# Performance work log

Measured on AMD Instinct MI355X. Metric: run time of the kernel, lower is better.

## Reference

```python
import jax, jax.numpy as jnp
import numpy as np

B, N_PIC, C, H, W, P = 32, 4, 3, 224, 224, 16
HP = H // P  # 14
NP = HP * HP  # 196 patches
D = C * P * P  # 768 = hidden_size


def setup_inputs() -> dict:
    key = jax.random.key(0)
    ks = jax.random.split(key, 12)
    s = 0.02
    def lin(k, din, dout):
        kw, kb = jax.random.split(k)
        return (jax.random.normal(kw, (din, dout), jnp.float32) * s,
                jax.random.normal(kb, (dout,), jnp.float32) * s)
    W1, b1 = lin(ks[0], D, D)
    Wq, bq = lin(ks[1], D, D)
    Wk, bk = lin(ks[2], D, D)
    Wv, bv = lin(ks[3], D, D)
    Wo1, bo1 = lin(ks[4], D, D)
    Wo2, bo2 = lin(ks[5], D, D)
    x = jax.random.normal(ks[6], (B, N_PIC, C, H, W), jnp.float32)
    return {"x": x, "W1": W1, "b1": b1, "Wq": Wq, "bq": bq, "Wk": Wk,
            "bk": bk, "Wv": Wv, "bv": bv, "Wo1": Wo1, "bo1": bo1,
            "Wo2": Wo2, "bo2": bo2}


def reference(x, W1, b1, Wq, bq, Wk, bk, Wv, bv, Wo1, bo1, Wo2, bo2):
    b = x.shape[0]
    # patchify: matches torch unfold(3,P,P).unfold(4,P,P) + permute + view
    # -> [b, N, num_patches, C*P*P] with (C, ph, pw) ordering in last dim
    p = x.reshape(b, N_PIC, C, HP, P, HP, P)
    p = p.transpose(0, 1, 3, 5, 2, 4, 6).reshape(b, N_PIC, NP, D)
    h = p @ W1 + b1  # [b, N, S, D]
    # attention: query always from picture 0; key/value per picture (batched)
    Q = h[:, 0] @ Wq + bq          # [b, S, D]
    K = h @ Wk + bk                # [b, N, S, D]
    V = h @ Wv + bv                # [b, N, S, D]
    scale = 1.0 / jnp.sqrt(jnp.float32(D))
    scores = jnp.einsum('bsd,bnmd->bnsm', Q, K) * scale  # [b, N, S, S]
    attn = jax.nn.softmax(scores, axis=-1)
    wv = jnp.einsum('bnsm,bnmd->bnsd', attn, V)           # [b, N, S, D]
    out = jax.nn.relu(wv @ Wo1 + bo1) @ Wo2 + bo2
    return out
```

## Files before the change

kernel.cpp:

```cpp
#include <hip/hip_runtime.h>

typedef __bf16 bf16;
typedef __bf16 bf16x8 __attribute__((ext_vector_type(8)));
typedef float  f32x4  __attribute__((ext_vector_type(4)));


__global__ __launch_bounds__(256) void patchify_k(const float* __restrict__ x,
                                                  bf16* __restrict__ p) {
  int t = blockIdx.x * 256 + threadIdx.x;
  if (t >= 128 * 3 * 14 * 16 * 14) return;
  int j  = t % 14; t /= 14;
  int ph = t % 16; t /= 16;
  int i  = t % 14; t /= 14;
  int c  = t % 3;  t /= 3;
  int bn = t;
  const float* src = x + (((long long)(bn * 3 + c) * 224 + (i * 16 + ph)) * 224 + j * 16);
  bf16* dst = p + ((long long)(bn * 196 + (i * 14 + j)) * 768 + c * 256 + ph * 16);
  bf16 tmp[16];
  for (int k = 0; k < 16; k += 4) {
    float4 f = *(const float4*)(src + k);
    tmp[k + 0] = (bf16)f.x; tmp[k + 1] = (bf16)f.y;
    tmp[k + 2] = (bf16)f.z; tmp[k + 3] = (bf16)f.w;
  }
  *(bf16x8*)(dst)     = *(bf16x8*)&tmp[0];
  *(bf16x8*)(dst + 8) = *(bf16x8*)&tmp[8];
}

__global__ __launch_bounds__(256) void wtrans_k(const float* __restrict__ w0,
                                                const float* __restrict__ w1,
                                                const float* __restrict__ w2,
                                                const float* __restrict__ w3,
                                                const float* __restrict__ w4,
                                                const float* __restrict__ w5,
                                                bf16* __restrict__ out) {
  __shared__ float tile[32][33];
  const float* W;
  switch (blockIdx.z) {
    case 0: W = w0; break; case 1: W = w1; break; case 2: W = w2; break;
    case 3: W = w3; break; case 4: W = w4; break; default: W = w5; break;
  }
  bf16* o = out + (long long)blockIdx.z * 768 * 768;
  int nb = blockIdx.x * 32, kb = blockIdx.y * 32;
  int c = threadIdx.x & 31, r = threadIdx.x >> 5;
  for (int rr = 0; rr < 32; rr += 8)
    tile[r + rr][c] = W[(long long)(kb + r + rr) * 768 + nb + c];
  __syncthreads();
  for (int rr = 0; rr < 32; rr += 8)
    o[(long long)(nb + r + rr) * 768 + kb + c] = (bf16)tile[c][r + rr];
}

__global__ __launch_bounds__(256) void vtrans_k(const bf16* __restrict__ kv,
                                                bf16* __restrict__ Vt) {
  __shared__ short tile[32][33];
  int z = blockIdx.z;
  const short* v = (const short*)(kv + (long long)z * 301056 + 768);
  short* vt = (short*)(Vt + (long long)z * 768 * 224);
  int db = blockIdx.x * 32;
  int mb = blockIdx.y * 32;
  int c = threadIdx.x & 31, r = threadIdx.x >> 5;
  for (int rr = 0; rr < 32; rr += 8) {
    int m = mb + r + rr;
    short val = 0;
    if (m < 196) val = v[(long long)m * 1536 + db + c];
    tile[r + rr][c] = val;
  }
  __syncthreads();
  for (int rr = 0; rr < 32; rr += 8) {
    int d = db + r + rr;
    vt[(long long)d * 224 + mb + c] = tile[c][r + rr];
  }
}

__global__ __launch_bounds__(64) void softmax_k(const float* __restrict__ S,
                                                bf16* __restrict__ attn) {
  const int row = blockIdx.x;
  const float* sr = S + (long long)row * 196;
  const int l = threadIdx.x;
  float v0 = sr[l];
  float v1 = sr[l + 64];
  float v2 = sr[l + 128];
  float v3 = (l + 192 < 196) ? sr[l + 192] : -1e30f;
  float mx = fmaxf(fmaxf(v0, v1), fmaxf(v2, v3));
  for (int o = 32; o > 0; o >>= 1) mx = fmaxf(mx, __shfl_xor(mx, o));
  float e0 = __expf(v0 - mx);
  float e1 = __expf(v1 - mx);
  float e2 = __expf(v2 - mx);
  float e3 = (l + 192 < 196) ? __expf(v3 - mx) : 0.f;
  float s = e0 + e1 + e2 + e3;
  for (int o = 32; o > 0; o >>= 1) s += __shfl_xor(s, o);
  float inv = 1.0f / s;
  bf16* ar = attn + (long long)row * 224;
  ar[l]       = (bf16)(e0 * inv);
  ar[l + 64]  = (bf16)(e1 * inv);
  ar[l + 128] = (bf16)(e2 * inv);
  int m3 = l + 192;
  if (m3 < 196) ar[m3] = (bf16)(e3 * inv);
  else if (m3 < 224) ar[m3] = (bf16)0.0f;
}

__device__ __forceinline__ void gld16(const bf16* g, bf16* l) {
  __builtin_amdgcn_global_load_lds(
      (const __attribute__((address_space(1))) unsigned int*)g,
      (__attribute__((address_space(3))) unsigned int*)l, 16, 0, 0);
}

__global__ __launch_bounds__(256) void gemm128(
    const bf16* __restrict__ A, const bf16* __restrict__ Bt,
    const float* __restrict__ bias, const float* __restrict__ bias2,
    void* __restrict__ Cout,
    int M, int N, int K, int lda, int ldb, int gr, long long gs,
    long long strideAz, int a_zdiv, long long strideBz, long long strideCz,
    float scale, int relu, int out_bf16) {
  __shared__ __align__(16) char smem[34816];
  bf16* AsBuf = (bf16*)smem;
  bf16* BsBuf = (bf16*)(smem + 16384);

  const int tid = threadIdx.x;
  const int lane = tid & 63;
  const int w = tid >> 6;
  const int wm = w & 1, wn = w >> 1;
  const int z = blockIdx.z;
  const int n0 = blockIdx.x * 128, m0 = blockIdx.y * 128;

  const bf16* Az  = A  + (long long)(z / a_zdiv) * strideAz;
  const bf16* Btz = Bt + (long long)z * strideBz;

  const int rl  = 16 * w + (lane & 15);
  const int kc8 = (lane >> 4) * 8;
  int ar0 = m0 + rl;        if (ar0 >= M) ar0 = M - 1;
  int ar1 = m0 + 64 + rl;   if (ar1 >= M) ar1 = M - 1;
  const bf16* aP0 = Az + (long long)(ar0 / gr) * gs + (long long)(ar0 % gr) * lda + kc8;
  const bf16* aP1 = Az + (long long)(ar1 / gr) * gs + (long long)(ar1 % gr) * lda + kc8;
  int br0 = n0 + rl;        if (br0 >= N) br0 = N - 1;
  int br1 = n0 + 64 + rl;   if (br1 >= N) br1 = N - 1;
  const bf16* bP0 = Btz + (long long)br0 * ldb + kc8;
  const bf16* bP1 = Btz + (long long)br1 * ldb + kc8;

  const int dstOff = w * 512;

#define ISSUE(t, buf) do { const int _o = (t) << 5;                 \
    gld16(aP0 + _o, AsBuf + (buf) * 4096 + dstOff);                 \
    gld16(aP1 + _o, AsBuf + (buf) * 4096 + 2048 + dstOff);          \
    gld16(bP0 + _o, BsBuf + (buf) * 4096 + dstOff);                 \
    gld16(bP1 + _o, BsBuf + (buf) * 4096 + 2048 + dstOff); } while (0)

  const int niter = K >> 5;
  f32x4 acc[4][4] = {};
  const int fr = lane & 15, fq = lane >> 4;

  ISSUE(0, 0);

  for (int i = 0; i < niter; ++i) {
    __syncthreads();
    const int cur = i & 1;
    if (i + 1 < niter) ISSUE(i + 1, cur ^ 1);

    const bf16* Ac = AsBuf + cur * 4096;
    const bf16* Bc = BsBuf + cur * 4096;
    bf16x8 a[4], b[4];
#pragma unroll
    for (int mi = 0; mi < 4; mi++)
      a[mi] = *(const bf16x8*)&Ac[(wm * 4 + mi) * 512 + fq * 128 + fr * 8];
#pragma unroll
    for (int ni = 0; ni < 4; ni++)
      b[ni] = *(const bf16x8*)&Bc[(wn * 4 + ni) * 512 + fq * 128 + fr * 8];
#pragma unroll
    for (int mi = 0; mi < 4; mi++)
#pragma unroll
      for (int ni = 0; ni < 4; ni++)
        acc[mi][ni] = __builtin_amdgcn_mfma_f32_16x16x32_bf16(a[mi], b[ni], acc[mi][ni], 0, 0, 0);
  }
#undef ISSUE

  __syncthreads();

  const long long cz = (long long)z * strideCz;
  if (out_bf16) {
    bf16* Cs = (bf16*)smem;
#pragma unroll
    for (int ni = 0; ni < 4; ni++) {
      int col = wn * 64 + ni * 16 + fr;
      int gcol = n0 + col;
      float bb = 0.f;
      if (bias) bb = (bias2 && gcol >= 768) ? bias2[gcol - 768] : bias[gcol];
#pragma unroll
      for (int mi = 0; mi < 4; mi++) {
        int rbase = wm * 64 + mi * 16 + fq * 4;
#pragma unroll
        for (int r = 0; r < 4; r++) {
          float v = acc[mi][ni][r] * scale + bb;
          if (relu) v = fmaxf(v, 0.f);
          Cs[(rbase + r) * 136 + col] = (bf16)v;
        }
      }
    }
    __syncthreads();
    bf16* Cp = (bf16*)Cout;
    const int rr = tid >> 4, cc = (tid & 15) * 8;
#pragma unroll
    for (int pp = 0; pp < 8; pp++) {
      int row = pp * 16 + rr;
      int grow = m0 + row;
      if (grow < M)
        *(bf16x8*)(Cp + cz + (long long)grow * N + n0 + cc) =
            *(const bf16x8*)&Cs[row * 136 + cc];
    }
  } else {
    float* Cs = (float*)smem;
    float* Cp = (float*)Cout;
    for (int half = 0; half < 2; ++half) {
      if (wm == half) {
#pragma unroll
        for (int ni = 0; ni < 4; ni++) {
          int col = wn * 64 + ni * 16 + fr;
          int gcol = n0 + col;
          float bb = 0.f;
          if (bias && gcol < N)
            bb = (bias2 && gcol >= 768) ? bias2[gcol - 768] : bias[gcol];
#pragma unroll
          for (int mi = 0; mi < 4; mi++) {
            int rbase = mi * 16 + fq * 4;
#pragma unroll
            for (int r = 0; r < 4; r++) {
              float v = acc[mi][ni][r] * scale + bb;
              if (relu) v = fmaxf(v, 0.f);
              Cs[(rbase + r) * 132 + col] = v;
            }
          }
        }
      }
      __syncthreads();
      const int rr = tid >> 5, cc = (tid & 31) * 4;
#pragma unroll
      for (int pp = 0; pp < 8; pp++) {
        int row = pp * 8 + rr;
        int grow = m0 + half * 64 + row;
        if (grow < M) {
          int gcol = n0 + cc;
          float* dst = Cp + cz + (long long)grow * N + gcol;
          const float* srcl = &Cs[row * 132 + cc];
          if (gcol + 4 <= N) {
            *(float4*)dst = *(const float4*)srcl;
          } else {
            for (int e = 0; e < 4; e++)
              if (gcol + e < N) dst[e] = srcl[e];
          }
        }
      }
      __syncthreads();
    }
  }
}

__global__ __launch_bounds__(512, 2) void gemm256(
    const bf16* __restrict__ A, const bf16* __restrict__ Bt,
    const float* __restrict__ bias, const float* __restrict__ bias2,
    void* __restrict__ Cout,
    int N, int K, int lda, int ldb, int relu, int out_bf16) {
  __shared__ __align__(16) char smem[131072];
  bf16* As = (bf16*)smem;
  bf16* Bs = (bf16*)(smem + 65536);

  const int tid = threadIdx.x;
  const int lane = tid & 63;
  const int w = tid >> 6;
  const int wm = w >> 2;
  const int wn = w & 3;

  const int nx = N >> 8;
  const int nwg = gridDim.x * gridDim.y;
  int f = blockIdx.y * gridDim.x + blockIdx.x;
  {
    const int q = nwg >> 3, r = nwg & 7;
    const int xcd = f & 7, idx = f >> 3;
    f = (xcd < r ? xcd * (q + 1) : r * (q + 1) + (xcd - r) * q) + idx;
  }
  const int n0 = (f % nx) * 256;
  const int m0 = (f / nx) * 256;

  const int srow = ((tid >> 2) & 15) + ((tid >> 7) << 4);
  const int scol = ((tid >> 6) & 1) * 32 +
                   (((tid & 3) << 3) ^ ((tid & 32) ? 16 : 0));
  const bf16* aBase = A  + (long long)(m0 + srow) * lda + scol;
  const bf16* bBase = Bt + (long long)(n0 + srow) * ldb + scol;
  const int ldsw = w * 512;

#define STGQ(base, ld, dstArr, buf, kt, hh, q)                               \
  gld16((base) + (long long)((hh) * 128 + (q) * 64) * (ld) + (kt) * 64,      \
        (dstArr) + (buf) * 16384 + (hh) * 8192 + (q) * 4096 + ldsw)

  const int fr = lane & 15, fq = lane >> 4;
  const int frij = fr * 32 + ((fq * 8) ^ ((fr & 8) ? 16 : 0));
  const bf16* aRd = As + wm * 8192 + frij;
  const bf16* bRd = Bs + (wn >> 1) * 8192 + (wn & 1) * 4096 + frij;

  f32x4 acc[8][4] = {};
  bf16x8 A0f[4][2], A1f[4][2], B0f[2][2], B1f[2][2];

  const int nt = K >> 6;

  STGQ(aBase, lda, As, 0, 0, 0, 0); STGQ(aBase, lda, As, 0, 0, 1, 0);
  STGQ(bBase, ldb, Bs, 0, 0, 1, 0); STGQ(bBase, ldb, Bs, 0, 0, 1, 1);
  STGQ(aBase, lda, As, 0, 0, 0, 1); STGQ(aBase, lda, As, 0, 0, 1, 1);
  STGQ(bBase, ldb, Bs, 0, 0, 0, 0); STGQ(bBase, ldb, Bs, 0, 0, 0, 1);
  STGQ(aBase, lda, As, 1, 1, 0, 0); STGQ(aBase, lda, As, 1, 1, 1, 0);
  STGQ(bBase, ldb, Bs, 1, 1, 1, 0); STGQ(bBase, ldb, Bs, 1, 1, 1, 1);
  STGQ(aBase, lda, As, 1, 1, 0, 1); STGQ(aBase, lda, As, 1, 1, 1, 1);
  STGQ(bBase, ldb, Bs, 1, 1, 0, 0); STGQ(bBase, ldb, Bs, 1, 1, 0, 1);
  asm volatile("s_waitcnt vmcnt(8)" ::: "memory");
  asm volatile("s_barrier" ::: "memory");
#pragma unroll
  for (int mi = 0; mi < 4; ++mi)
#pragma unroll
    for (int kk = 0; kk < 2; ++kk)
      A0f[mi][kk] = *(const bf16x8*)(aRd + mi * 1024 + kk * 512);
#pragma unroll
  for (int ni = 0; ni < 2; ++ni)
#pragma unroll
    for (int kk = 0; kk < 2; ++kk)
      B0f[ni][kk] = *(const bf16x8*)(bRd + ni * 1024 + kk * 512);
  asm volatile("s_waitcnt lgkmcnt(0)" ::: "memory");
  __builtin_amdgcn_sched_barrier(0);
  asm volatile("s_barrier" ::: "memory");

  for (int t = 0; t < nt; ++t) {
    const int bo = (t & 1) << 14;
    const int bn = ((t & 1) ^ 1) << 14;
    const int b = t & 1;
    const bool stg = (t + 2 < nt);
    const bool nxt = (t + 1 < nt);

#pragma unroll
    for (int ni = 0; ni < 2; ++ni)
#pragma unroll
      for (int kk = 0; kk < 2; ++kk)
        B1f[ni][kk] = *(const bf16x8*)(bRd + bo + (2 + ni) * 1024 + kk * 512);
    if (stg) { STGQ(aBase, lda, As, b, t + 2, 0, 0);
               STGQ(aBase, lda, As, b, t + 2, 1, 0); }
    asm volatile("s_barrier" ::: "memory");
    __builtin_amdgcn_s_setprio(1);
#pragma unroll
    for (int mi = 0; mi < 4; ++mi)
#pragma unroll
      for (int ni = 0; ni < 2; ++ni)
#pragma unroll
        for (int kk = 0; kk < 2; ++kk)
          acc[mi][ni] = __builtin_amdgcn_mfma_f32_16x16x32_bf16(
              A0f[mi][kk], B0f[ni][kk], acc[mi][ni], 0, 0, 0);
    __builtin_amdgcn_s_setprio(0);
    asm volatile("s_barrier" ::: "memory");

#pragma unroll
    for (int mi = 0; mi < 4; ++mi)
#pragma unroll
      for (int kk = 0; kk < 2; ++kk)
        A1f[mi][kk] = *(const bf16x8*)(aRd + bo + (4 + mi) * 1024 + kk * 512);
    if (stg) { STGQ(bBase, ldb, Bs, b, t + 2, 1, 0);
               STGQ(bBase, ldb, Bs, b, t + 2, 1, 1); }
    asm volatile("s_barrier" ::: "memory");
    __builtin_amdgcn_s_setprio(1);
#pragma unroll
    for (int mi = 0; mi < 4; ++mi)
#pragma unroll
      for (int ni = 0; ni < 2; ++ni)
#pragma unroll
        for (int kk = 0; kk < 2; ++kk)
          acc[mi][2 + ni] = __builtin_amdgcn_mfma_f32_16x16x32_bf16(
              A0f[mi][kk], B1f[ni][kk], acc[mi][2 + ni], 0, 0, 0);
    __builtin_amdgcn_s_setprio(0);
    if (stg) asm volatile("s_waitcnt vmcnt(6)" ::: "memory");
    else     asm volatile("s_waitcnt vmcnt(2)" ::: "memory");
    asm volatile("s_barrier" ::: "memory");

    if (nxt) {
#pragma unroll
      for (int mi = 0; mi < 4; ++mi)
#pragma unroll
        for (int kk = 0; kk < 2; ++kk)
          A0f[mi][kk] = *(const bf16x8*)(aRd + bn + mi * 1024 + kk * 512);
    }
    if (stg) { STGQ(aBase, lda, As, b, t + 2, 0, 1);
               STGQ(aBase, lda, As, b, t + 2, 1, 1); }
    asm volatile("s_barrier" ::: "memory");
    __builtin_amdgcn_s_setprio(1);
#pragma unroll
    for (int mi = 0; mi < 4; ++mi)
#pragma unroll
      for (int ni = 0; ni < 2; ++ni)
#pragma unroll
        for (int kk = 0; kk < 2; ++kk)
          acc[4 + mi][ni] = __builtin_amdgcn_mfma_f32_16x16x32_bf16(
              A1f[mi][kk], B0f[ni][kk], acc[4 + mi][ni], 0, 0, 0);
    __builtin_amdgcn_s_setprio(0);
    if (stg) asm volatile("s_waitcnt vmcnt(6)" ::: "memory");
    else     asm volatile("s_waitcnt vmcnt(0)" ::: "memory");
    asm volatile("s_barrier" ::: "memory");

    if (nxt) {
#pragma unroll
      for (int ni = 0; ni < 2; ++ni)
#pragma unroll
        for (int kk = 0; kk < 2; ++kk)
          B0f[ni][kk] = *(const bf16x8*)(bRd + bn + ni * 1024 + kk * 512);
    }
    if (stg) { STGQ(bBase, ldb, Bs, b, t + 2, 0, 0);
               STGQ(bBase, ldb, Bs, b, t + 2, 0, 1); }
    asm volatile("s_barrier" ::: "memory");
    __builtin_amdgcn_s_setprio(1);
#pragma unroll
    for (int mi = 0; mi < 4; ++mi)
#pragma unroll
      for (int ni = 0; ni < 2; ++ni)
#pragma unroll
        for (int kk = 0; kk < 2; ++kk)
          acc[4 + mi][2 + ni] = __builtin_amdgcn_mfma_f32_16x16x32_bf16(
              A1f[mi][kk], B1f[ni][kk], acc[4 + mi][2 + ni], 0, 0, 0);
    __builtin_amdgcn_s_setprio(0);
    asm volatile("s_barrier" ::: "memory");
  }
#undef STGQ

  const long long Nll = N;
  if (out_bf16) {
    bf16* Cs = (bf16*)smem;
    bf16* Cp = (bf16*)Cout;
#pragma unroll
    for (int half = 0; half < 2; ++half) {
      if (wm == half) {
#pragma unroll
        for (int ni = 0; ni < 4; ++ni) {
          const int col = wn * 64 + ni * 16 + fr;
          const int gcol = n0 + col;
          float bb = 0.f;
          if (bias) bb = (bias2 && gcol >= 768) ? bias2[gcol - 768] : bias[gcol];
#pragma unroll
          for (int mi = 0; mi < 8; ++mi) {
#pragma unroll
            for (int r = 0; r < 4; ++r) {
              float v = acc[mi][ni][r] + bb;
              if (relu) v = fmaxf(v, 0.f);
              Cs[(mi * 16 + fq * 4 + r) * 268 + col] = (bf16)v;
            }
          }
        }
      }
      __syncthreads();
      const int row = tid >> 2, cb = (tid & 3) * 8;
      const bf16* srcl = &Cs[row * 268 + cb];
      bf16* dst = Cp + (long long)(m0 + half * 128 + row) * Nll + n0 + cb;
#pragma unroll
      for (int j = 0; j < 8; ++j)
        *(bf16x8*)(dst + j * 32) = *(const bf16x8*)(srcl + j * 32);
      __syncthreads();
    }
  } else {
    float* Cs = (float*)smem;
    float* Cp = (float*)Cout;
#pragma unroll
    for (int pass = 0; pass < 4; ++pass) {
      if (wm == (pass >> 1)) {
#pragma unroll
        for (int ni = 0; ni < 4; ++ni) {
          const int col = wn * 64 + ni * 16 + fr;
          const int gcol = n0 + col;
          float bb = 0.f;
          if (bias) bb = (bias2 && gcol >= 768) ? bias2[gcol - 768] : bias[gcol];
#pragma unroll
          for (int mi2 = 0; mi2 < 4; ++mi2) {
            const int mi = (pass & 1) * 4 + mi2;
#pragma unroll
            for (int r = 0; r < 4; ++r) {
              float v = acc[mi][ni][r] + bb;
              if (relu) v = fmaxf(v, 0.f);
              Cs[(mi2 * 16 + fq * 4 + r) * 268 + col] = v;
            }
          }
        }
      }
      __syncthreads();
      const int row = tid >> 3, c4 = (tid & 7) * 4;
      const float* srcl = &Cs[row * 268 + c4];
      float* dst = Cp + (long long)(m0 + pass * 64 + row) * Nll + n0 + c4;
#pragma unroll
      for (int j = 0; j < 8; ++j)
        *(float4*)(dst + j * 32) = *(const float4*)(srcl + j * 32);
      __syncthreads();
    }
  }
}

extern "C" void kernel_launch(void* const* d_in, const int* in_sizes, int n_in,
                              void* d_out, int out_size, void* d_ws, size_t ws_size,
                              hipStream_t stream) {
  (void)in_sizes; (void)n_in; (void)out_size; (void)ws_size;
  const float* x   = (const float*)d_in[0];
  const float* W1  = (const float*)d_in[1];
  const float* b1  = (const float*)d_in[2];
  const float* Wq  = (const float*)d_in[3];
  const float* bq  = (const float*)d_in[4];
  const float* Wk  = (const float*)d_in[5];
  const float* bk  = (const float*)d_in[6];
  const float* Wv  = (const float*)d_in[7];
  const float* bv  = (const float*)d_in[8];
  const float* Wo1 = (const float*)d_in[9];
  const float* bo1 = (const float*)d_in[10];
  const float* Wo2 = (const float*)d_in[11];
  const float* bo2 = (const float*)d_in[12];

  char* ws = (char*)d_ws;
  bf16*  p    = (bf16*)(ws + 0);
  bf16*  vt   = (bf16*)(ws + 0);
  bf16*  h    = (bf16*)(ws + 44040192LL);
  bf16*  wv   = (bf16*)(ws + 44040192LL);
  bf16*  kv   = (bf16*)(ws + 82575360LL);
  bf16*  o1   = (bf16*)(ws + 82575360LL);
  float* sc   = (float*)(ws + 159645696LL);
  bf16*  q    = (bf16*)(ws + 179314688LL);
  bf16*  attn = (bf16*)(ws + 179314688LL);
  bf16*  wt   = (bf16*)(ws + 190554112LL);
  constexpr long long WSZ = 768LL * 768;

  const float qk_scale = 0.03608439182435161f;

  patchify_k<<<4704, 256, 0, stream>>>(x, p);
  wtrans_k<<<dim3(24, 24, 6), 256, 0, stream>>>(W1, Wk, Wv, Wq, Wo1, Wo2, wt);

  gemm256<<<dim3(3, 98), 512, 0, stream>>>(p, wt + 0 * WSZ, b1, nullptr, h,
      768, 768, 768, 768, 0, 1);
  gemm256<<<dim3(6, 98), 512, 0, stream>>>(h, wt + 1 * WSZ, bk, bv, kv,
      1536, 768, 768, 768, 0, 1);
  gemm128<<<dim3(6, 49, 1), 256, 0, stream>>>(h, wt + 3 * WSZ, bq, nullptr, q,
      6272, 768, 768, 768, 768, 196, 602112LL, 0LL, 1, 0LL, 0LL, 1.f, 0, 1);
  vtrans_k<<<dim3(24, 7, 128), 256, 0, stream>>>(kv, vt);
  gemm128<<<dim3(2, 2, 128), 256, 0, stream>>>(q, kv, nullptr, nullptr, sc,
      196, 196, 768, 768, 1536, 196, 0LL, 150528LL, 4, 301056LL, 38416LL,
      qk_scale, 0, 0);
  softmax_k<<<25088, 64, 0, stream>>>(sc, attn);
  gemm128<<<dim3(6, 2, 128), 256, 0, stream>>>(attn, vt, nullptr, nullptr, wv,
      196, 768, 224, 224, 224, 196, 0LL, 43904LL, 1, 172032LL, 150528LL,
      1.f, 0, 1);
  gemm256<<<dim3(3, 98), 512, 0, stream>>>(wv, wt + 4 * WSZ, bo1, nullptr, o1,
      768, 768, 768, 768, 1, 1);
  gemm256<<<dim3(3, 98), 512, 0, stream>>>(o1, wt + 5 * WSZ, bo2, nullptr,
      (float*)d_out, 768, 768, 768, 768, 0, 0);
}
```

Baseline: 560.0 us.

## Switch gemm256 to 32x32x16 MFMA tiles and batch softmax rows per block

```diff
diff --git a/kernel.cpp b/kernel.cpp
--- a/kernel.cpp
+++ b/kernel.cpp
@@ -3,6 +3,7 @@
 typedef __bf16 bf16;
 typedef __bf16 bf16x8 __attribute__((ext_vector_type(8)));
 typedef float  f32x4  __attribute__((ext_vector_type(4)));
+typedef float  f32x16 __attribute__((ext_vector_type(16)));
 
 
 __global__ __launch_bounds__(256) void patchify_k(const float* __restrict__ x,
@@ -71,11 +72,11 @@
   }
 }
 
-__global__ __launch_bounds__(64) void softmax_k(const float* __restrict__ S,
-                                                bf16* __restrict__ attn) {
-  const int row = blockIdx.x;
+__global__ __launch_bounds__(256) void softmax_k(const float* __restrict__ S,
+                                                 bf16* __restrict__ attn) {
+  const int row = blockIdx.x * 4 + (threadIdx.x >> 6);
   const float* sr = S + (long long)row * 196;
-  const int l = threadIdx.x;
+  const int l = threadIdx.x & 63;
   float v0 = sr[l];
   float v1 = sr[l + 64];
   float v2 = sr[l + 128];
@@ -289,133 +290,111 @@
   gld16((base) + (long long)((hh) * 128 + (q) * 64) * (ld) + (kt) * 64,      \
         (dstArr) + (buf) * 16384 + (hh) * 8192 + (q) * 4096 + ldsw)
 
-  const int fr = lane & 15, fq = lane >> 4;
-  const int frij = fr * 32 + ((fq * 8) ^ ((fr & 8) ? 16 : 0));
-  const bf16* aRd = As + wm * 8192 + frij;
-  const bf16* bRd = Bs + (wn >> 1) * 8192 + (wn & 1) * 4096 + frij;
-
-  f32x4 acc[8][4] = {};
-  bf16x8 A0f[4][2], A1f[4][2], B0f[2][2], B1f[2][2];
+  const int l15 = lane & 15, l31 = lane & 31;
+  const int lh = (lane >> 4) & 1;
+  const int lq = lane >> 5;
+  const int swz0 = (l15 & 8) ? 16 : 0;
+  const int e0 = (lq * 8) ^ swz0;
+  const int e1 = (16 + lq * 8) ^ swz0;
+  const int rdb = lh * 1024 + l15 * 32;
+  const bf16* aRd = As + wm * 8192 + rdb;
+  const bf16* bRd = Bs + (wn >> 1) * 8192 + (wn & 1) * 4096 + rdb;
+
+  f32x16 acc[4][2] = {};
+  bf16x8 aF[2][4], B0f[4], B1f[4];
 
   const int nt = K >> 6;
 
   STGQ(aBase, lda, As, 0, 0, 0, 0); STGQ(aBase, lda, As, 0, 0, 1, 0);
+  STGQ(bBase, ldb, Bs, 0, 0, 0, 0); STGQ(bBase, ldb, Bs, 0, 0, 0, 1);
   STGQ(bBase, ldb, Bs, 0, 0, 1, 0); STGQ(bBase, ldb, Bs, 0, 0, 1, 1);
   STGQ(aBase, lda, As, 0, 0, 0, 1); STGQ(aBase, lda, As, 0, 0, 1, 1);
-  STGQ(bBase, ldb, Bs, 0, 0, 0, 0); STGQ(bBase, ldb, Bs, 0, 0, 0, 1);
-  STGQ(aBase, lda, As, 1, 1, 0, 0); STGQ(aBase, lda, As, 1, 1, 1, 0);
-  STGQ(bBase, ldb, Bs, 1, 1, 1, 0); STGQ(bBase, ldb, Bs, 1, 1, 1, 1);
-  STGQ(aBase, lda, As, 1, 1, 0, 1); STGQ(aBase, lda, As, 1, 1, 1, 1);
-  STGQ(bBase, ldb, Bs, 1, 1, 0, 0); STGQ(bBase, ldb, Bs, 1, 1, 0, 1);
+  if (nt > 1) {
+    STGQ(aBase, lda, As, 1, 1, 0, 0); STGQ(aBase, lda, As, 1, 1, 1, 0);
+    STGQ(bBase, ldb, Bs, 1, 1, 0, 0); STGQ(bBase, ldb, Bs, 1, 1, 0, 1);
+    STGQ(bBase, ldb, Bs, 1, 1, 1, 0); STGQ(bBase, ldb, Bs, 1, 1, 1, 1);
+    STGQ(aBase, lda, As, 1, 1, 0, 1); STGQ(aBase, lda, As, 1, 1, 1, 1);
+  }
   asm volatile("s_waitcnt vmcnt(8)" ::: "memory");
   asm volatile("s_barrier" ::: "memory");
-#pragma unroll
-  for (int mi = 0; mi < 4; ++mi)
-#pragma unroll
-    for (int kk = 0; kk < 2; ++kk)
-      A0f[mi][kk] = *(const bf16x8*)(aRd + mi * 1024 + kk * 512);
-#pragma unroll
-  for (int ni = 0; ni < 2; ++ni)
-#pragma unroll
-    for (int kk = 0; kk < 2; ++kk)
-      B0f[ni][kk] = *(const bf16x8*)(bRd + ni * 1024 + kk * 512);
-  asm volatile("s_waitcnt lgkmcnt(0)" ::: "memory");
-  __builtin_amdgcn_sched_barrier(0);
-  asm volatile("s_barrier" ::: "memory");
 
   for (int t = 0; t < nt; ++t) {
     const int bo = (t & 1) << 14;
-    const int bn = ((t & 1) ^ 1) << 14;
     const int b = t & 1;
     const bool stg = (t + 2 < nt);
-    const bool nxt = (t + 1 < nt);
-
-#pragma unroll
-    for (int ni = 0; ni < 2; ++ni)
-#pragma unroll
-      for (int kk = 0; kk < 2; ++kk)
-        B1f[ni][kk] = *(const bf16x8*)(bRd + bo + (2 + ni) * 1024 + kk * 512);
+
+#pragma unroll
+    for (int m = 0; m < 2; ++m)
+#pragma unroll
+      for (int ks = 0; ks < 4; ++ks)
+        aF[m][ks] = *(const bf16x8*)(aRd + bo + m * 2048 + (ks >> 1) * 512 +
+                                     ((ks & 1) ? e1 : e0));
+#pragma unroll
+    for (int ks = 0; ks < 4; ++ks)
+      B0f[ks] = *(const bf16x8*)(bRd + bo + (ks >> 1) * 512 +
+                                 ((ks & 1) ? e1 : e0));
+    asm volatile("s_barrier" ::: "memory");
+    __builtin_amdgcn_s_setprio(1);
+#pragma unroll
+    for (int ks = 0; ks < 4; ++ks)
+#pragma unroll
+      for (int m = 0; m < 2; ++m)
+        acc[m][0] = __builtin_amdgcn_mfma_f32_32x32x16_bf16(
+            aF[m][ks], B0f[ks], acc[m][0], 0, 0, 0);
+    __builtin_amdgcn_s_setprio(0);
+    asm volatile("s_barrier" ::: "memory");
+
+#pragma unroll
+    for (int ks = 0; ks < 4; ++ks)
+      B1f[ks] = *(const bf16x8*)(bRd + bo + 2048 + (ks >> 1) * 512 +
+                                 ((ks & 1) ? e1 : e0));
     if (stg) { STGQ(aBase, lda, As, b, t + 2, 0, 0);
                STGQ(aBase, lda, As, b, t + 2, 1, 0); }
     asm volatile("s_barrier" ::: "memory");
     __builtin_amdgcn_s_setprio(1);
 #pragma unroll
-    for (int mi = 0; mi < 4; ++mi)
-#pragma unroll
-      for (int ni = 0; ni < 2; ++ni)
-#pragma unroll
-        for (int kk = 0; kk < 2; ++kk)
-          acc[mi][ni] = __builtin_amdgcn_mfma_f32_16x16x32_bf16(
-              A0f[mi][kk], B0f[ni][kk], acc[mi][ni], 0, 0, 0);
+    for (int ks = 0; ks < 4; ++ks)
+#pragma unroll
+      for (int m = 0; m < 2; ++m)
+        acc[m][1] = __builtin_amdgcn_mfma_f32_32x32x16_bf16(
+            aF[m][ks], B1f[ks], acc[m][1], 0, 0, 0);
     __builtin_amdgcn_s_setprio(0);
     asm volatile("s_barrier" ::: "memory");
 
 #pragma unroll
-    for (int mi = 0; mi < 4; ++mi)
-#pragma unroll
-      for (int kk = 0; kk < 2; ++kk)
-        A1f[mi][kk] = *(const bf16x8*)(aRd + bo + (4 + mi) * 1024 + kk * 512);
-    if (stg) { STGQ(bBase, ldb, Bs, b, t + 2, 1, 0);
+    for (int m = 0; m < 2; ++m)
+#pragma unroll
+      for (int ks = 0; ks < 4; ++ks)
+        aF[m][ks] = *(const bf16x8*)(aRd + bo + (2 + m) * 2048 + (ks >> 1) * 512 +
+                                     ((ks & 1) ? e1 : e0));
+    if (stg) { STGQ(bBase, ldb, Bs, b, t + 2, 0, 0);
+               STGQ(bBase, ldb, Bs, b, t + 2, 0, 1);
+               STGQ(bBase, ldb, Bs, b, t + 2, 1, 0);
                STGQ(bBase, ldb, Bs, b, t + 2, 1, 1); }
     asm volatile("s_barrier" ::: "memory");
     __builtin_amdgcn_s_setprio(1);
 #pragma unroll
-    for (int mi = 0; mi < 4; ++mi)
-#pragma unroll
-      for (int ni = 0; ni < 2; ++ni)
-#pragma unroll
-        for (int kk = 0; kk < 2; ++kk)
-          acc[mi][2 + ni] = __builtin_amdgcn_mfma_f32_16x16x32_bf16(
-              A0f[mi][kk], B1f[ni][kk], acc[mi][2 + ni], 0, 0, 0);
+    for (int ks = 0; ks < 4; ++ks)
+#pragma unroll
+      for (int m = 0; m < 2; ++m)
+        acc[2 + m][0] = __builtin_amdgcn_mfma_f32_32x32x16_bf16(
+            aF[m][ks], B0f[ks], acc[2 + m][0], 0, 0, 0);
     __builtin_amdgcn_s_setprio(0);
-    if (stg) asm volatile("s_waitcnt vmcnt(6)" ::: "memory");
-    else     asm volatile("s_waitcnt vmcnt(2)" ::: "memory");
-    asm volatile("s_barrier" ::: "memory");
-
-    if (nxt) {
-#pragma unroll
-      for (int mi = 0; mi < 4; ++mi)
-#pragma unroll
-        for (int kk = 0; kk < 2; ++kk)
-          A0f[mi][kk] = *(const bf16x8*)(aRd + bn + mi * 1024 + kk * 512);
-    }
+    asm volatile("s_barrier" ::: "memory");
+
     if (stg) { STGQ(aBase, lda, As, b, t + 2, 0, 1);
                STGQ(aBase, lda, As, b, t + 2, 1, 1); }
     asm volatile("s_barrier" ::: "memory");
     __builtin_amdgcn_s_setprio(1);
 #pragma unroll
-    for (int mi = 0; mi < 4; ++mi)
-#pragma unroll
-      for (int ni = 0; ni < 2; ++ni)
-#pragma unroll
-        for (int kk = 0; kk < 2; ++kk)
-          acc[4 + mi][ni] = __builtin_amdgcn_mfma_f32_16x16x32_bf16(
-              A1f[mi][kk], B0f[ni][kk], acc[4 + mi][ni], 0, 0, 0);
+    for (int ks = 0; ks < 4; ++ks)
+#pragma unroll
+      for (int m = 0; m < 2; ++m)
+        acc[2 + m][1] = __builtin_amdgcn_mfma_f32_32x32x16_bf16(
+            aF[m][ks], B1f[ks], acc[2 + m][1], 0, 0, 0);
     __builtin_amdgcn_s_setprio(0);
-    if (stg) asm volatile("s_waitcnt vmcnt(6)" ::: "memory");
+    if (stg) asm volatile("s_waitcnt vmcnt(8)" ::: "memory");
     else     asm volatile("s_waitcnt vmcnt(0)" ::: "memory");
-    asm volatile("s_barrier" ::: "memory");
-
-    if (nxt) {
-#pragma unroll
-      for (int ni = 0; ni < 2; ++ni)
-#pragma unroll
-        for (int kk = 0; kk < 2; ++kk)
-          B0f[ni][kk] = *(const bf16x8*)(bRd + bn + ni * 1024 + kk * 512);
-    }
-    if (stg) { STGQ(bBase, ldb, Bs, b, t + 2, 0, 0);
-               STGQ(bBase, ldb, Bs, b, t + 2, 0, 1); }
-    asm volatile("s_barrier" ::: "memory");
-    __builtin_amdgcn_s_setprio(1);
-#pragma unroll
-    for (int mi = 0; mi < 4; ++mi)
-#pragma unroll
-      for (int ni = 0; ni < 2; ++ni)
-#pragma unroll
-        for (int kk = 0; kk < 2; ++kk)
-          acc[4 + mi][2 + ni] = __builtin_amdgcn_mfma_f32_16x16x32_bf16(
-              A1f[mi][kk], B1f[ni][kk], acc[4 + mi][2 + ni], 0, 0, 0);
-    __builtin_amdgcn_s_setprio(0);
     asm volatile("s_barrier" ::: "memory");
   }
 #undef STGQ
@@ -428,18 +407,19 @@
     for (int half = 0; half < 2; ++half) {
       if (wm == half) {
 #pragma unroll
-        for (int ni = 0; ni < 4; ++ni) {
-          const int col = wn * 64 + ni * 16 + fr;
+        for (int n2 = 0; n2 < 2; ++n2) {
+          const int col = wn * 64 + n2 * 32 + l31;
           const int gcol = n0 + col;
           float bb = 0.f;
           if (bias) bb = (bias2 && gcol >= 768) ? bias2[gcol - 768] : bias[gcol];
 #pragma unroll
-          for (int mi = 0; mi < 8; ++mi) {
-#pragma unroll
-            for (int r = 0; r < 4; ++r) {
-              float v = acc[mi][ni][r] + bb;
+          for (int m2 = 0; m2 < 4; ++m2) {
+#pragma unroll
+            for (int reg = 0; reg < 16; ++reg) {
+              const int row = m2 * 32 + (reg & 3) + 8 * (reg >> 2) + 4 * lq;
+              float v = acc[m2][n2][reg] + bb;
               if (relu) v = fmaxf(v, 0.f);
-              Cs[(mi * 16 + fq * 4 + r) * 268 + col] = (bf16)v;
+              Cs[row * 268 + col] = (bf16)v;
             }
           }
         }
@@ -460,19 +440,20 @@
     for (int pass = 0; pass < 4; ++pass) {
       if (wm == (pass >> 1)) {
 #pragma unroll
-        for (int ni = 0; ni < 4; ++ni) {
-          const int col = wn * 64 + ni * 16 + fr;
+        for (int n2 = 0; n2 < 2; ++n2) {
+          const int col = wn * 64 + n2 * 32 + l31;
           const int gcol = n0 + col;
           float bb = 0.f;
           if (bias) bb = (bias2 && gcol >= 768) ? bias2[gcol - 768] : bias[gcol];
 #pragma unroll
-          for (int mi2 = 0; mi2 < 4; ++mi2) {
-            const int mi = (pass & 1) * 4 + mi2;
-#pragma unroll
-            for (int r = 0; r < 4; ++r) {
-              float v = acc[mi][ni][r] + bb;
+          for (int mh = 0; mh < 2; ++mh) {
+            const int m2 = (pass & 1) * 2 + mh;
+#pragma unroll
+            for (int reg = 0; reg < 16; ++reg) {
+              const int row = mh * 32 + (reg & 3) + 8 * (reg >> 2) + 4 * lq;
+              float v = acc[m2][n2][reg] + bb;
               if (relu) v = fmaxf(v, 0.f);
-              Cs[(mi2 * 16 + fq * 4 + r) * 268 + col] = v;
+              Cs[row * 268 + col] = v;
             }
           }
         }
@@ -535,7 +516,7 @@
   gemm128<<<dim3(2, 2, 128), 256, 0, stream>>>(q, kv, nullptr, nullptr, sc,
       196, 196, 768, 768, 1536, 196, 0LL, 150528LL, 4, 301056LL, 38416LL,
       qk_scale, 0, 0);
-  softmax_k<<<25088, 64, 0, stream>>>(sc, attn);
+  softmax_k<<<6272, 256, 0, stream>>>(sc, attn);
   gemm128<<<dim3(6, 2, 128), 256, 0, stream>>>(attn, vt, nullptr, nullptr, wv,
       196, 768, 224, 224, 224, 196, 0LL, 43904LL, 1, 172032LL, 150528LL,
       1.f, 0, 1);
```

New measurement: 574.8 us. 1.03x slower.

## Fuse patchify into first GEMM A-loads and pack four softmax rows per block

Applied to the files above, without the earlier changes.

```diff
diff --git a/kernel.cpp b/kernel.cpp
--- a/kernel.cpp
+++ b/kernel.cpp
@@ -4,27 +4,6 @@
 typedef __bf16 bf16x8 __attribute__((ext_vector_type(8)));
 typedef float  f32x4  __attribute__((ext_vector_type(4)));
 
-
-__global__ __launch_bounds__(256) void patchify_k(const float* __restrict__ x,
-                                                  bf16* __restrict__ p) {
-  int t = blockIdx.x * 256 + threadIdx.x;
-  if (t >= 128 * 3 * 14 * 16 * 14) return;
-  int j  = t % 14; t /= 14;
-  int ph = t % 16; t /= 16;
-  int i  = t % 14; t /= 14;
-  int c  = t % 3;  t /= 3;
-  int bn = t;
-  const float* src = x + (((long long)(bn * 3 + c) * 224 + (i * 16 + ph)) * 224 + j * 16);
-  bf16* dst = p + ((long long)(bn * 196 + (i * 14 + j)) * 768 + c * 256 + ph * 16);
-  bf16 tmp[16];
-  for (int k = 0; k < 16; k += 4) {
-    float4 f = *(const float4*)(src + k);
-    tmp[k + 0] = (bf16)f.x; tmp[k + 1] = (bf16)f.y;
-    tmp[k + 2] = (bf16)f.z; tmp[k + 3] = (bf16)f.w;
-  }
-  *(bf16x8*)(dst)     = *(bf16x8*)&tmp[0];
-  *(bf16x8*)(dst + 8) = *(bf16x8*)&tmp[8];
-}
 
 __global__ __launch_bounds__(256) void wtrans_k(const float* __restrict__ w0,
                                                 const float* __restrict__ w1,
@@ -71,11 +50,11 @@
   }
 }
 
-__global__ __launch_bounds__(64) void softmax_k(const float* __restrict__ S,
-                                                bf16* __restrict__ attn) {
-  const int row = blockIdx.x;
+__global__ __launch_bounds__(256) void softmax_k(const float* __restrict__ S,
+                                                 bf16* __restrict__ attn) {
+  const int row = blockIdx.x * 4 + (threadIdx.x >> 6);
   const float* sr = S + (long long)row * 196;
-  const int l = threadIdx.x;
+  const int l = threadIdx.x & 63;
   float v0 = sr[l];
   float v1 = sr[l + 64];
   float v2 = sr[l + 128];
@@ -489,6 +468,223 @@
   }
 }
 
+__global__ __launch_bounds__(512, 2) void gemm256_px(
+    const float* __restrict__ x, const bf16* __restrict__ Bt,
+    const float* __restrict__ bias,
+    void* __restrict__ Cout,
+    int N, int K, int ldb, int relu) {
+  __shared__ __align__(16) char smem[131072];
+  bf16* As = (bf16*)smem;
+  bf16* Bs = (bf16*)(smem + 65536);
+
+  const int tid = threadIdx.x;
+  const int lane = tid & 63;
+  const int w = tid >> 6;
+  const int wm = w >> 2;
+  const int wn = w & 3;
+
+  const int nx = N >> 8;
+  const int nwg = gridDim.x * gridDim.y;
+  int f = blockIdx.y * gridDim.x + blockIdx.x;
+  {
+    const int q = nwg >> 3, r = nwg & 7;
+    const int xcd = f & 7, idx = f >> 3;
+    f = (xcd < r ? xcd * (q + 1) : r * (q + 1) + (xcd - r) * q) + idx;
+  }
+  const int n0 = (f % nx) * 256;
+  const int m0 = (f / nx) * 256;
+
+  const int srow = ((tid >> 2) & 15) + ((tid >> 7) << 4);
+  const int scol = ((tid >> 6) & 1) * 32 +
+                   (((tid & 3) << 3) ^ ((tid & 32) ? 16 : 0));
+  const bf16* bBase = Bt + (long long)(n0 + srow) * ldb + scol;
+  const int ldsw = w * 512;
+
+  const float* xrb[4];
+#pragma unroll
+  for (int hh = 0; hh < 2; ++hh)
+#pragma unroll
+    for (int qq = 0; qq < 2; ++qq) {
+      int m = m0 + srow + hh * 128 + qq * 64;
+      int bn = m / 196, pt = m % 196;
+      int i = pt / 14, j = pt % 14;
+      xrb[hh * 2 + qq] = x + (long long)bn * 150528 + (i * 16) * 224 + j * 16;
+    }
+
+#define ASTG(buf, kt, hh, qq) do {                                            \
+    const int _c8 = (kt) * 64 + scol;                                         \
+    const float* _s = xrb[(hh) * 2 + (qq)] + (_c8 >> 8) * 50176 +             \
+                      ((_c8 >> 4) & 15) * 224 + (_c8 & 15);                   \
+    float4 _f0 = *(const float4*)_s; float4 _f1 = *(const float4*)(_s + 4);   \
+    bf16x8 _v;                                                                \
+    _v[0] = (bf16)_f0.x; _v[1] = (bf16)_f0.y;                                 \
+    _v[2] = (bf16)_f0.z; _v[3] = (bf16)_f0.w;                                 \
+    _v[4] = (bf16)_f1.x; _v[5] = (bf16)_f1.y;                                 \
+    _v[6] = (bf16)_f1.z; _v[7] = (bf16)_f1.w;                                 \
+    *(bf16x8*)(As + (buf) * 16384 + (hh) * 8192 + (qq) * 4096 + ldsw +        \
+               lane * 8) = _v;                                                \
+  } while (0)
+
+#define STGB(buf, kt, hh, qq)                                                 \
+  gld16(bBase + (long long)((hh) * 128 + (qq) * 64) * ldb + (kt) * 64,        \
+        Bs + (buf) * 16384 + (hh) * 8192 + (qq) * 4096 + ldsw)
+
+  const int fr = lane & 15, fq = lane >> 4;
+  const int frij = fr * 32 + ((fq * 8) ^ ((fr & 8) ? 16 : 0));
+  const bf16* aRd = As + wm * 8192 + frij;
+  const bf16* bRd = Bs + (wn >> 1) * 8192 + (wn & 1) * 4096 + frij;
+
+  f32x4 acc[8][4] = {};
+  bf16x8 A0f[4][2], A1f[4][2], B0f[2][2], B1f[2][2];
+
+  const int nt = K >> 6;
+
+  ASTG(0, 0, 0, 0); ASTG(0, 0, 1, 0); ASTG(0, 0, 0, 1); ASTG(0, 0, 1, 1);
+  ASTG(1, 1, 0, 0); ASTG(1, 1, 1, 0); ASTG(1, 1, 0, 1); ASTG(1, 1, 1, 1);
+  STGB(0, 0, 1, 0); STGB(0, 0, 1, 1); STGB(0, 0, 0, 0); STGB(0, 0, 0, 1);
+  STGB(1, 1, 1, 0); STGB(1, 1, 1, 1); STGB(1, 1, 0, 0); STGB(1, 1, 0, 1);
+  asm volatile("s_waitcnt vmcnt(4)" ::: "memory");
+  asm volatile("s_waitcnt lgkmcnt(0)" ::: "memory");
+  asm volatile("s_barrier" ::: "memory");
+#pragma unroll
+  for (int mi = 0; mi < 4; ++mi)
+#pragma unroll
+    for (int kk = 0; kk < 2; ++kk)
+      A0f[mi][kk] = *(const bf16x8*)(aRd + mi * 1024 + kk * 512);
+#pragma unroll
+  for (int ni = 0; ni < 2; ++ni)
+#pragma unroll
+    for (int kk = 0; kk < 2; ++kk)
+      B0f[ni][kk] = *(const bf16x8*)(bRd + ni * 1024 + kk * 512);
+  asm volatile("s_waitcnt lgkmcnt(0)" ::: "memory");
+  __builtin_amdgcn_sched_barrier(0);
+  asm volatile("s_barrier" ::: "memory");
+
+  for (int t = 0; t < nt; ++t) {
+    const int bo = (t & 1) << 14;
+    const int bn = ((t & 1) ^ 1) << 14;
+    const int b = t & 1;
+    const bool stg = (t + 2 < nt);
+    const bool nxt = (t + 1 < nt);
+
+#pragma unroll
+    for (int ni = 0; ni < 2; ++ni)
+#pragma unroll
+      for (int kk = 0; kk < 2; ++kk)
+        B1f[ni][kk] = *(const bf16x8*)(bRd + bo + (2 + ni) * 1024 + kk * 512);
+    asm volatile("s_barrier" ::: "memory");
+    __builtin_amdgcn_s_setprio(1);
+#pragma unroll
+    for (int mi = 0; mi < 4; ++mi)
+#pragma unroll
+      for (int ni = 0; ni < 2; ++ni)
+#pragma unroll
+        for (int kk = 0; kk < 2; ++kk)
+          acc[mi][ni] = __builtin_amdgcn_mfma_f32_16x16x32_bf16(
+              A0f[mi][kk], B0f[ni][kk], acc[mi][ni], 0, 0, 0);
+    __builtin_amdgcn_s_setprio(0);
+    asm volatile("s_barrier" ::: "memory");
+
+#pragma unroll
+    for (int mi = 0; mi < 4; ++mi)
+#pragma unroll
+      for (int kk = 0; kk < 2; ++kk)
+        A1f[mi][kk] = *(const bf16x8*)(aRd + bo + (4 + mi) * 1024 + kk * 512);
+    if (stg) { ASTG(b, t + 2, 0, 0); ASTG(b, t + 2, 1, 0);
+               STGB(b, t + 2, 1, 0); STGB(b, t + 2, 1, 1); }
+    asm volatile("s_barrier" ::: "memory");
+    __builtin_amdgcn_s_setprio(1);
+#pragma unroll
+    for (int mi = 0; mi < 4; ++mi)
+#pragma unroll
+      for (int ni = 0; ni < 2; ++ni)
+#pragma unroll
+        for (int kk = 0; kk < 2; ++kk)
+          acc[mi][2 + ni] = __builtin_amdgcn_mfma_f32_16x16x32_bf16(
+              A0f[mi][kk], B1f[ni][kk], acc[mi][2 + ni], 0, 0, 0);
+    __builtin_amdgcn_s_setprio(0);
+    asm volatile("s_barrier" ::: "memory");
+
+    if (nxt) {
+#pragma unroll
+      for (int mi = 0; mi < 4; ++mi)
+#pragma unroll
+        for (int kk = 0; kk < 2; ++kk)
+          A0f[mi][kk] = *(const bf16x8*)(aRd + bn + mi * 1024 + kk * 512);
+    }
+    asm volatile("s_barrier" ::: "memory");
+    __builtin_amdgcn_s_setprio(1);
+#pragma unroll
+    for (int mi = 0; mi < 4; ++mi)
+#pragma unroll
+      for (int ni = 0; ni < 2; ++ni)
+#pragma unroll
+        for (int kk = 0; kk < 2; ++kk)
+          acc[4 + mi][ni] = __builtin_amdgcn_mfma_f32_16x16x32_bf16(
+              A1f[mi][kk], B0f[ni][kk], acc[4 + mi][ni], 0, 0, 0);
+    __builtin_amdgcn_s_setprio(0);
+    if (stg) asm volatile("s_waitcnt vmcnt(2)" ::: "memory");
+    else     asm volatile("s_waitcnt vmcnt(0)" ::: "memory");
+    asm volatile("s_barrier" ::: "memory");
+
+    if (nxt) {
+#pragma unroll
+      for (int ni = 0; ni < 2; ++ni)
+#pragma unroll
+        for (int kk = 0; kk < 2; ++kk)
+          B0f[ni][kk] = *(const bf16x8*)(bRd + bn + ni * 1024 + kk * 512);
+    }
+    if (stg) { ASTG(b, t + 2, 0, 1); ASTG(b, t + 2, 1, 1);
+               STGB(b, t + 2, 0, 0); STGB(b, t + 2, 0, 1); }
+    asm volatile("s_barrier" ::: "memory");
+    __builtin_amdgcn_s_setprio(1);
+#pragma unroll
+    for (int mi = 0; mi < 4; ++mi)
+#pragma unroll
+      for (int ni = 0; ni < 2; ++ni)
+#pragma unroll
+        for (int kk = 0; kk < 2; ++kk)
+          acc[4 + mi][2 + ni] = __builtin_amdgcn_mfma_f32_16x16x32_bf16(
+              A1f[mi][kk], B1f[ni][kk], acc[4 + mi][2 + ni], 0, 0, 0);
+    __builtin_amdgcn_s_setprio(0);
+    asm volatile("s_barrier" ::: "memory");
+  }
+#undef ASTG
+#undef STGB
+
+  const long long Nll = N;
+  bf16* Cs = (bf16*)smem;
+  bf16* Cp = (bf16*)Cout;
+#pragma unroll
+  for (int half = 0; half < 2; ++half) {
+    if (wm == half) {
+#pragma unroll
+      for (int ni = 0; ni < 4; ++ni) {
+        const int col = wn * 64 + ni * 16 + fr;
+        const int gcol = n0 + col;
+        float bb = bias ? bias[gcol] : 0.f;
+#pragma unroll
+        for (int mi = 0; mi < 8; ++mi) {
+#pragma unroll
+          for (int r = 0; r < 4; ++r) {
+            float v = acc[mi][ni][r] + bb;
+            if (relu) v = fmaxf(v, 0.f);
+            Cs[(mi * 16 + fq * 4 + r) * 268 + col] = (bf16)v;
+          }
+        }
+      }
+    }
+    __syncthreads();
+    const int row = tid >> 2, cb = (tid & 3) * 8;
+    const bf16* srcl = &Cs[row * 268 + cb];
+    bf16* dst = Cp + (long long)(m0 + half * 128 + row) * Nll + n0 + cb;
+#pragma unroll
+    for (int j = 0; j < 8; ++j)
+      *(bf16x8*)(dst + j * 32) = *(const bf16x8*)(srcl + j * 32);
+    __syncthreads();
+  }
+}
+
 extern "C" void kernel_launch(void* const* d_in, const int* in_sizes, int n_in,
                               void* d_out, int out_size, void* d_ws, size_t ws_size,
                               hipStream_t stream) {
@@ -508,7 +704,6 @@
   const float* bo2 = (const float*)d_in[12];
 
   char* ws = (char*)d_ws;
-  bf16*  p    = (bf16*)(ws + 0);
   bf16*  vt   = (bf16*)(ws + 0);
   bf16*  h    = (bf16*)(ws + 44040192LL);
   bf16*  wv   = (bf16*)(ws + 44040192LL);
@@ -522,11 +717,10 @@
 
   const float qk_scale = 0.03608439182435161f;
 
-  patchify_k<<<4704, 256, 0, stream>>>(x, p);
   wtrans_k<<<dim3(24, 24, 6), 256, 0, stream>>>(W1, Wk, Wv, Wq, Wo1, Wo2, wt);
 
-  gemm256<<<dim3(3, 98), 512, 0, stream>>>(p, wt + 0 * WSZ, b1, nullptr, h,
-      768, 768, 768, 768, 0, 1);
+  gemm256_px<<<dim3(3, 98), 512, 0, stream>>>(x, wt + 0 * WSZ, b1, h,
+      768, 768, 768, 0);
   gemm256<<<dim3(6, 98), 512, 0, stream>>>(h, wt + 1 * WSZ, bk, bv, kv,
       1536, 768, 768, 768, 0, 1);
   gemm128<<<dim3(6, 49, 1), 256, 0, stream>>>(h, wt + 3 * WSZ, bq, nullptr, q,
@@ -535,7 +729,7 @@
   gemm128<<<dim3(2, 2, 128), 256, 0, stream>>>(q, kv, nullptr, nullptr, sc,
       196, 196, 768, 768, 1536, 196, 0LL, 150528LL, 4, 301056LL, 38416LL,
       qk_scale, 0, 0);
-  softmax_k<<<25088, 64, 0, stream>>>(sc, attn);
+  softmax_k<<<6272, 256, 0, stream>>>(sc, attn);
   gemm128<<<dim3(6, 2, 128), 256, 0, stream>>>(attn, vt, nullptr, nullptr, wv,
       196, 768, 224, 224, 224, 196, 0LL, 43904LL, 1, 172032LL, 150528LL,
       1.f, 0, 1);
```

Result: slower. 600.8 us (+7.3%).
